# Optimization experiments

Measured on AMD Instinct MI355X. Metric: run time of the kernel, lower is better.

Reference implementation:

```python
import jax, jax.numpy as jnp
import numpy as np

NUM_NODES = 256
INPUTS = list(range(8))
OUTPUTS = list(range(248, 256))
V_MEAS = np.array(sorted(set(range(NUM_NODES)) - set(OUTPUTS)))  # 0..247
V_CORR = np.array(sorted(set(range(NUM_NODES)) - set(INPUTS)))   # 8..255
INNER_LR = 0.1
INNER_ITER = 200
B1, B2, ADAM_EPS = 0.9, 0.999, 1e-8
CAUSAL_EPS = 0.1


def _parity_loss(G, A_sub):
    # G, A_sub: [B, m, c]; enforces sum(A*G) odd
    S = jnp.sum(A_sub * G, axis=2)                 # [B, m]
    val = jnp.sin(jnp.pi * S / 2) ** 2
    return jnp.mean((val - 1.0) ** 2)


def _causal_loss(G, T):
    # T: [B, n]; penalty = relu(T_u - T_v + eps)
    T_u = T[:, V_MEAS][:, :, None]                 # [B, m, 1]
    T_v = T[:, V_CORR][:, None, :]                 # [B, 1, c]
    penalty = jax.nn.relu(T_u - T_v + CAUSAL_EPS)  # [B, m, c]
    return jnp.mean(G * penalty)


def setup_inputs() -> dict:
    key = jax.random.key(0)
    k1, k2, k3 = jax.random.split(key, 3)
    B = 128
    adj_batch = jax.random.uniform(k1, (B, NUM_NODES, NUM_NODES), dtype=jnp.float32)
    G_logits0 = jax.random.normal(k2, (B, len(V_MEAS), len(V_CORR)), dtype=jnp.float32)
    T0 = jax.random.uniform(k3, (B, NUM_NODES), dtype=jnp.float32)
    return {"adj_batch": adj_batch, "G_logits0": G_logits0, "T0": T0}


def reference(adj_batch, G_logits0, T0):
    A_sub = adj_batch[:, V_MEAS][:, :, V_CORR]     # [B, m, c]
    A_det = jax.lax.stop_gradient(A_sub)           # adj is detached in the inner loop

    def inner_loss(params):
        G_logits, T = params
        G = jax.nn.sigmoid(G_logits)
        loss_p = _parity_loss(G, A_det)
        loss_c = _causal_loss(G, T)
        loss_s = jnp.mean(jnp.abs(G - 0.5)) * 0.1
        return loss_p + loss_c + loss_s

    grad_fn = jax.grad(inner_loss)

    def adam_step(carry, t):
        params, m, v = carry
        g = grad_fn(params)
        m = jax.tree.map(lambda m_, g_: B1 * m_ + (1 - B1) * g_, m, g)
        v = jax.tree.map(lambda v_, g_: B2 * v_ + (1 - B2) * g_ * g_, v, g)
        bc1 = 1.0 - B1 ** t
        bc2 = 1.0 - B2 ** t
        params = jax.tree.map(
            lambda p, m_, v_: p - INNER_LR * (m_ / bc1) / (jnp.sqrt(v_ / bc2) + ADAM_EPS),
            params, m, v)
        return (params, m, v), None

    params0 = (G_logits0, T0)
    zeros = jax.tree.map(jnp.zeros_like, params0)
    steps = jnp.arange(1, INNER_ITER + 1, dtype=jnp.float32)
    (params, _, _), _ = jax.lax.scan(adam_step, (params0, zeros, zeros), steps)

    G_logits, T = jax.lax.stop_gradient(params)    # .detach() in torch source
    G_final = jax.nn.sigmoid(G_logits)
    final_parity = _parity_loss(G_final, A_sub)    # differentiable w.r.t. adj_batch
    final_causal = _causal_loss(G_final, T)
    return (final_parity + final_causal, final_parity, final_causal)
```

## Files before the change

kernel.cpp:

```cpp
#include <hip/hip_runtime.h>
#include <hip/hip_cooperative_groups.h>
#include <math.h>

namespace cg = cooperative_groups;

#define B_N   128
#define M_N   248
#define C_N   248
#define NODES 256
#define NT    (B_N*NODES)
#define NG    (B_N*M_N*C_N)

#define GRID  256
#define TPB   512
#define HROWS 124
#define KMAX  16

#define PI_F     3.14159265358979323846f
#define INV_BM   (1.0f/31744.0f)
#define INV_BMC  (1.0f/7872512.0f)

__device__ __forceinline__ float sigm(float x) {
    float z = expf(-fabsf(x));
    return (x >= 0.0f) ? 1.0f/(1.0f+z) : z/(1.0f+z);
}
__device__ __forceinline__ float sgn(float x) {
    return (x > 0.0f) ? 1.0f : ((x < 0.0f) ? -1.0f : 0.0f);
}

__global__ __launch_bounds__(TPB, 2) void persist_kernel(
    const float* __restrict__ adj, const float* __restrict__ Gl0,
    const float* __restrict__ T0,
    float* __restrict__ gTu,
    float* __restrict__ gTv,
    float* __restrict__ accum,
    float* __restrict__ out)
{
    __shared__ float T_lds[NODES], mT_lds[NODES], vT_lds[NODES];
    __shared__ float red[16];

    cg::grid_group grid = cg::this_grid();
    const int tid  = threadIdx.x;
    const int blkI = blockIdx.x;
    const int b    = blkI >> 1;
    const int h    = blkI & 1;
    const int wave = tid >> 6, lane = tid & 63;
    const int j0 = lane, j1 = lane+64, j2 = lane+128, j3 = lane+192;
    const bool v3 = (lane < 56);

    if (tid < NODES) {
        T_lds[tid]  = T0[b*NODES + tid];
        mT_lds[tid] = 0.0f;
        vT_lds[tid] = 0.0f;
    }

    float Gr[KMAX][4], mGr[KMAX][4], vGr[KMAX][4];
    #pragma unroll
    for (int k = 0; k < KMAX; ++k) {
        #pragma unroll
        for (int s = 0; s < 4; ++s) { Gr[k][s]=0.0f; mGr[k][s]=0.0f; vGr[k][s]=0.0f; }
        const int lr = wave + 8*k;
        if (lr < HROWS) {
            const int i = h*HROWS + lr;
            const size_t grow = ((size_t)(b*M_N + i))*C_N;
            Gr[k][0] = Gl0[grow+j0];
            Gr[k][1] = Gl0[grow+j1];
            Gr[k][2] = Gl0[grow+j2];
            if (v3) Gr[k][3] = Gl0[grow+j3];
        }
    }
    __syncthreads();

    double pw1d = 1.0, pw2d = 1.0;
    #pragma unroll 1
    for (int t = 1; t <= 200; ++t) {
        const float bc1p = (float)(1.0 - pw1d), bc2p = (float)(1.0 - pw2d);
        pw1d *= 0.9; pw2d *= 0.999;
        const float bc1 = (float)(1.0 - pw1d), bc2 = (float)(1.0 - pw2d);
        const int pw = t & 1, ps = (t-1) & 1;

        if (t > 1) {
            grid.sync();
            if (tid < NODES) {
                float g = 0.0f;
                if (tid < M_N) g += gTu[ps*(B_N*M_N) + b*M_N + tid];
                if (tid >= 8) {
                    const float* gp = gTv + (size_t)ps*(GRID*8*256)
                                    + (size_t)(b*16)*256 + (tid-8);
                    float s = 0.0f;
                    #pragma unroll
                    for (int p = 0; p < 16; ++p) s += gp[p*256];
                    g -= s;
                }
                g *= INV_BMC;
                float m_ = 0.9f*mT_lds[tid] + 0.1f*g;
                float v_ = 0.999f*vT_lds[tid] + 0.001f*(g*g);
                mT_lds[tid] = m_; vT_lds[tid] = v_;
                T_lds[tid] = T_lds[tid] - 0.1f*(m_/bc1p)/(sqrtf(v_/bc2p) + 1e-8f);
            }
            __syncthreads();
        }

        float av0 = 0.0f, av1 = 0.0f, av2 = 0.0f, av3 = 0.0f;
        #pragma unroll
        for (int k = 0; k < KMAX; ++k) {
            const int lr = wave + 8*k;
            if (lr < HROWS) {
                const int i = h*HROWS + lr;
                const size_t arow = ((size_t)(b*NODES + i))*NODES + 8;
                const float a0 = adj[arow+j0];
                const float a1 = adj[arow+j1];
                const float a2 = adj[arow+j2];
                const float a3 = v3 ? adj[arow+j3] : 0.0f;

                const float G0 = sigm(Gr[k][0]), G1 = sigm(Gr[k][1]);
                const float G2 = sigm(Gr[k][2]), G3 = sigm(Gr[k][3]);

                const float Tu = T_lds[i];
                const float d0 = Tu - T_lds[j0+8] + 0.1f;
                const float d1 = Tu - T_lds[j1+8] + 0.1f;
                const float d2 = Tu - T_lds[j2+8] + 0.1f;
                const float d3 = v3 ? (Tu - T_lds[j3+8] + 0.1f) : 0.0f;
                const float p0 = fmaxf(d0,0.0f), p1 = fmaxf(d1,0.0f);
                const float p2 = fmaxf(d2,0.0f), p3 = fmaxf(d3,0.0f);
                const float mk0 = (d0>0.0f)?1.0f:0.0f;
                const float mk1 = (d1>0.0f)?1.0f:0.0f;
                const float mk2 = (d2>0.0f)?1.0f:0.0f;
                const float mk3 = (v3 && d3>0.0f)?1.0f:0.0f;

                float sp = a0*G0 + a1*G1 + a2*G2 + (v3 ? a3*G3 : 0.0f);
                float gu = G0*mk0 + G1*mk1 + G2*mk2 + G3*mk3;
                #pragma unroll
                for (int off = 32; off > 0; off >>= 1) {
                    sp += __shfl_xor(sp, off, 64);
                    gu += __shfl_xor(gu, off, 64);
                }
                av0 += G0*mk0; av1 += G1*mk1; av2 += G2*mk2; av3 += G3*mk3;

                const float half_arg = (PI_F*sp)*0.5f;
                const float sv = sinf(half_arg), cv = cosf(half_arg);
                const float coefP = 2.0f*(sv*sv-1.0f)*sv*cv*PI_F*INV_BM;

                if (lane == 0) gTu[pw*(B_N*M_N) + b*M_N + i] = gu;

                #define DO_SLOT(Gx, ax, px, s_, valid) do { if (valid) {                 \
                    float dG  = coefP*(ax) + (px)*INV_BMC + 0.1f*INV_BMC*sgn((Gx)-0.5f); \
                    float grd = dG * (Gx) * (1.0f - (Gx));                               \
                    float m_ = 0.9f*mGr[k][s_] + 0.1f*grd;                               \
                    float v_ = 0.999f*vGr[k][s_] + 0.001f*(grd*grd);                     \
                    mGr[k][s_] = m_; vGr[k][s_] = v_;                                    \
                    Gr[k][s_] = Gr[k][s_] - 0.1f*(m_/bc1)/(sqrtf(v_/bc2)+1e-8f);         \
                } } while (0)
                DO_SLOT(G0, a0, p0, 0, true);
                DO_SLOT(G1, a1, p1, 1, true);
                DO_SLOT(G2, a2, p2, 2, true);
                DO_SLOT(G3, a3, p3, 3, v3);
                #undef DO_SLOT
            }
        }
        {
            float* gpw = gTv + (size_t)pw*(GRID*8*256) + (size_t)(blkI*8 + wave)*256;
            gpw[j0] = av0; gpw[j1] = av1; gpw[j2] = av2; gpw[j3] = av3;
        }
    }

    grid.sync();
    if (tid < NODES) {
        const float bc1p = (float)(1.0 - pw1d), bc2p = (float)(1.0 - pw2d);
        float g = 0.0f;
        if (tid < M_N) g += gTu[0*(B_N*M_N) + b*M_N + tid];
        if (tid >= 8) {
            const float* gp = gTv + (size_t)(b*16)*256 + (tid-8);
            float s = 0.0f;
            #pragma unroll
            for (int p = 0; p < 16; ++p) s += gp[p*256];
            g -= s;
        }
        g *= INV_BMC;
        float m_ = 0.9f*mT_lds[tid] + 0.1f*g;
        float v_ = 0.999f*vT_lds[tid] + 0.001f*(g*g);
        T_lds[tid] = T_lds[tid] - 0.1f*(m_/bc1p)/(sqrtf(v_/bc2p) + 1e-8f);
    }
    __syncthreads();

    float pacc = 0.0f, cacc = 0.0f;
    #pragma unroll
    for (int k = 0; k < KMAX; ++k) {
        const int lr = wave + 8*k;
        if (lr < HROWS) {
            const int i = h*HROWS + lr;
            const size_t arow = ((size_t)(b*NODES + i))*NODES + 8;
            const float a0 = adj[arow+j0];
            const float a1 = adj[arow+j1];
            const float a2 = adj[arow+j2];
            const float a3 = v3 ? adj[arow+j3] : 0.0f;
            const float G0 = sigm(Gr[k][0]), G1 = sigm(Gr[k][1]);
            const float G2 = sigm(Gr[k][2]), G3 = sigm(Gr[k][3]);
            const float Tu = T_lds[i];
            const float p0 = fmaxf(Tu - T_lds[j0+8] + 0.1f, 0.0f);
            const float p1 = fmaxf(Tu - T_lds[j1+8] + 0.1f, 0.0f);
            const float p2 = fmaxf(Tu - T_lds[j2+8] + 0.1f, 0.0f);
            const float p3 = v3 ? fmaxf(Tu - T_lds[j3+8] + 0.1f, 0.0f) : 0.0f;

            float sp = a0*G0 + a1*G1 + a2*G2 + (v3 ? a3*G3 : 0.0f);
            float cp = G0*p0 + G1*p1 + G2*p2 + (v3 ? G3*p3 : 0.0f);
            #pragma unroll
            for (int off = 32; off > 0; off >>= 1) {
                sp += __shfl_xor(sp, off, 64);
                cp += __shfl_xor(cp, off, 64);
            }
            if (lane == 0) {
                const float sv = sinf((PI_F*sp)*0.5f);
                const float dd = sv*sv - 1.0f;
                pacc += dd*dd;
                cacc += cp;
            }
        }
    }
    if (lane == 0) { red[wave] = pacc; red[8+wave] = cacc; }
    __syncthreads();
    if (tid == 0) {
        float rp = 0.0f, rc = 0.0f;
        #pragma unroll
        for (int w = 0; w < 8; ++w) { rp += red[w]; rc += red[8+w]; }
        atomicAdd(&accum[0], rp);
        atomicAdd(&accum[1], rc);
    }
    __threadfence();
    grid.sync();
    if (blkI == 0 && tid == 0) {
        const float p = __hip_atomic_load(&accum[0], __ATOMIC_RELAXED, __HIP_MEMORY_SCOPE_AGENT) * INV_BM;
        const float c = __hip_atomic_load(&accum[1], __ATOMIC_RELAXED, __HIP_MEMORY_SCOPE_AGENT) * INV_BMC;
        out[0] = p + c;
        out[1] = p;
        out[2] = c;
    }
}

#define NBLK  8
#define RPB   31

__global__ __launch_bounds__(256) void iter_kernel(
    const float* __restrict__ adj, float* __restrict__ Gl,
    float* __restrict__ mG, float* __restrict__ vG,
    float* __restrict__ T_state, float* __restrict__ mT, float* __restrict__ vT,
    float* __restrict__ gTu, float* __restrict__ gTv,
    int t, float bc1p, float bc2p, float bc1, float bc2)
{
    __shared__ float T_lds[NODES];
    __shared__ float gv_lds[4*NODES];
    const int tid = threadIdx.x;
    const int b   = blockIdx.x >> 3;
    const int blk = blockIdx.x & 7;

    if (t == 1) {
        T_lds[tid] = T_state[b*NODES + tid];
    } else {
        const int rs = t & 1, ws2 = (t+1) & 1, ps = (t-1) & 1;
        const int idx = b*NODES + tid;
        float Tval = T_state[rs*NT + idx];
        float g = 0.0f;
        if (tid < M_N) g += gTu[ps*(B_N*M_N) + b*M_N + tid];
        if (tid >= 8) {
            const float* gp = gTv + (size_t)ps*(B_N*NBLK*C_N) + (size_t)b*NBLK*C_N + (tid-8);
            float s = 0.0f;
            #pragma unroll
            for (int k = 0; k < NBLK; ++k) s += gp[k*C_N];
            g -= s;
        }
        g *= INV_BMC;
        float m_ = 0.9f*mT[rs*NT+idx] + 0.1f*g;
        float v_ = 0.999f*vT[rs*NT+idx] + 0.001f*(g*g);
        float newT = Tval - 0.1f*(m_/bc1p)/(sqrtf(v_/bc2p) + 1e-8f);
        T_state[ws2*NT+idx] = newT;
        mT[ws2*NT+idx] = m_;
        vT[ws2*NT+idx] = v_;
        T_lds[tid] = newT;
    }
    gv_lds[tid] = 0.0f; gv_lds[256+tid] = 0.0f; gv_lds[512+tid] = 0.0f; gv_lds[768+tid] = 0.0f;
    __syncthreads();

    const int wave = tid >> 6, lane = tid & 63;
    const int pw = t & 1;
    const int j0 = lane, j1 = lane+64, j2 = lane+128, j3 = lane+192;
    const bool v3 = (lane < 56);
    float av0 = 0.0f, av1 = 0.0f, av2 = 0.0f, av3 = 0.0f;

    for (int r = wave; r < RPB; r += 4) {
        const int i = blk*RPB + r;
        const size_t arow = ((size_t)(b*NODES + i))*NODES + 8;
        const size_t grow = ((size_t)(b*M_N + i))*C_N;

        float gl0 = Gl[grow+j0], gl1 = Gl[grow+j1], gl2 = Gl[grow+j2];
        float gl3 = v3 ? Gl[grow+j3] : 0.0f;
        float a0 = adj[arow+j0], a1 = adj[arow+j1], a2 = adj[arow+j2];
        float a3 = v3 ? adj[arow+j3] : 0.0f;
        float G0 = sigm(gl0), G1 = sigm(gl1), G2 = sigm(gl2), G3 = sigm(gl3);

        float Tu = T_lds[i];
        float d0 = Tu - T_lds[j0+8] + 0.1f;
        float d1 = Tu - T_lds[j1+8] + 0.1f;
        float d2 = Tu - T_lds[j2+8] + 0.1f;
        float d3 = v3 ? (Tu - T_lds[j3+8] + 0.1f) : 0.0f;
        float p0 = fmaxf(d0, 0.0f), p1 = fmaxf(d1, 0.0f);
        float p2 = fmaxf(d2, 0.0f), p3 = fmaxf(d3, 0.0f);
        float mk0 = (d0 > 0.0f) ? 1.0f : 0.0f;
        float mk1 = (d1 > 0.0f) ? 1.0f : 0.0f;
        float mk2 = (d2 > 0.0f) ? 1.0f : 0.0f;
        float mk3 = (v3 && d3 > 0.0f) ? 1.0f : 0.0f;

        float sp = a0*G0 + a1*G1 + a2*G2 + (v3 ? a3*G3 : 0.0f);
        float gu = G0*mk0 + G1*mk1 + G2*mk2 + G3*mk3;
        #pragma unroll
        for (int off = 32; off > 0; off >>= 1) {
            sp += __shfl_xor(sp, off, 64);
            gu += __shfl_xor(gu, off, 64);
        }
        av0 += G0*mk0; av1 += G1*mk1; av2 += G2*mk2; av3 += G3*mk3;

        float half_arg = (PI_F*sp)*0.5f;
        float sv = sinf(half_arg), cv = cosf(half_arg);
        float val = sv*sv;
        float coefP = 2.0f*(val-1.0f)*sv*cv*PI_F*INV_BM;

        if (lane == 0) gTu[pw*(B_N*M_N) + b*M_N + i] = gu;

        #define DO_SLOT(Gx, glx, ax, px, jx, valid) do { if (valid) {            \
            float dG  = coefP*(ax) + (px)*INV_BMC + 0.1f*INV_BMC*sgn((Gx)-0.5f); \
            float grd = dG * (Gx) * (1.0f - (Gx));                               \
            float m_ = 0.9f*mG[grow+(jx)] + 0.1f*grd;                            \
            float v_ = 0.999f*vG[grow+(jx)] + 0.001f*(grd*grd);                  \
            mG[grow+(jx)] = m_; vG[grow+(jx)] = v_;                              \
            Gl[grow+(jx)] = (glx) - 0.1f*(m_/bc1)/(sqrtf(v_/bc2)+1e-8f);         \
        } } while (0)
        DO_SLOT(G0, gl0, a0, p0, j0, true);
        DO_SLOT(G1, gl1, a1, p1, j1, true);
        DO_SLOT(G2, gl2, a2, p2, j2, true);
        DO_SLOT(G3, gl3, a3, p3, j3, v3);
        #undef DO_SLOT
    }

    gv_lds[wave*256 + j0] = av0;
    gv_lds[wave*256 + j1] = av1;
    gv_lds[wave*256 + j2] = av2;
    if (v3) gv_lds[wave*256 + j3] = av3;
    __syncthreads();
    if (tid < C_N) {
        float s = gv_lds[tid] + gv_lds[256+tid] + gv_lds[512+tid] + gv_lds[768+tid];
        gTv[(size_t)pw*(B_N*NBLK*C_N) + (size_t)(b*NBLK + blk)*C_N + tid] = s;
    }
}

__global__ __launch_bounds__(256) void t_fin_kernel(
    float* __restrict__ T_state, const float* __restrict__ mT, const float* __restrict__ vT,
    const float* __restrict__ gTu, const float* __restrict__ gTv,
    float bc1p, float bc2p)
{
    const int b = blockIdx.x, tid = threadIdx.x;
    const int idx = b*NODES + tid;
    float Tval = T_state[1*NT + idx];
    float g = 0.0f;
    if (tid < M_N) g += gTu[0*(B_N*M_N) + b*M_N + tid];
    if (tid >= 8) {
        const float* gp = gTv + (size_t)b*NBLK*C_N + (tid-8);
        float s = 0.0f;
        #pragma unroll
        for (int k = 0; k < NBLK; ++k) s += gp[k*C_N];
        g -= s;
    }
    g *= INV_BMC;
    float m_ = 0.9f*mT[1*NT+idx] + 0.1f*g;
    float v_ = 0.999f*vT[1*NT+idx] + 0.001f*(g*g);
    T_state[0*NT+idx] = Tval - 0.1f*(m_/bc1p)/(sqrtf(v_/bc2p) + 1e-8f);
}

__global__ __launch_bounds__(256) void loss_kernel(
    const float* __restrict__ adj, const float* __restrict__ Gl,
    const float* __restrict__ T_state, float* __restrict__ accum)
{
    __shared__ float T_lds[NODES];
    __shared__ float red[8];
    const int tid = threadIdx.x;
    const int b = blockIdx.x >> 3, blk = blockIdx.x & 7;
    T_lds[tid] = T_state[b*NODES + tid];
    __syncthreads();
    const int wave = tid >> 6, lane = tid & 63;
    const int j0 = lane, j1 = lane+64, j2 = lane+128, j3 = lane+192;
    const bool v3 = (lane < 56);
    float pacc = 0.0f, cacc = 0.0f;

    for (int r = wave; r < RPB; r += 4) {
        const int i = blk*RPB + r;
        const size_t arow = ((size_t)(b*NODES + i))*NODES + 8;
        const size_t grow = ((size_t)(b*M_N + i))*C_N;
        float gl0 = Gl[grow+j0], gl1 = Gl[grow+j1], gl2 = Gl[grow+j2];
        float gl3 = v3 ? Gl[grow+j3] : 0.0f;
        float a0 = adj[arow+j0], a1 = adj[arow+j1], a2 = adj[arow+j2];
        float a3 = v3 ? adj[arow+j3] : 0.0f;
        float G0 = sigm(gl0), G1 = sigm(gl1), G2 = sigm(gl2), G3 = sigm(gl3);

        float Tu = T_lds[i];
        float p0 = fmaxf(Tu - T_lds[j0+8] + 0.1f, 0.0f);
        float p1 = fmaxf(Tu - T_lds[j1+8] + 0.1f, 0.0f);
        float p2 = fmaxf(Tu - T_lds[j2+8] + 0.1f, 0.0f);
        float p3 = v3 ? fmaxf(Tu - T_lds[j3+8] + 0.1f, 0.0f) : 0.0f;

        float sp = a0*G0 + a1*G1 + a2*G2 + (v3 ? a3*G3 : 0.0f);
        float cp = G0*p0 + G1*p1 + G2*p2 + (v3 ? G3*p3 : 0.0f);
        #pragma unroll
        for (int off = 32; off > 0; off >>= 1) {
            sp += __shfl_xor(sp, off, 64);
            cp += __shfl_xor(cp, off, 64);
        }
        if (lane == 0) {
            float sv = sinf((PI_F*sp)*0.5f);
            float dd = sv*sv - 1.0f;
            pacc += dd*dd;
            cacc += cp;
        }
    }
    if (lane == 0) { red[wave] = pacc; red[4+wave] = cacc; }
    __syncthreads();
    if (tid == 0) {
        atomicAdd(&accum[0], red[0]+red[1]+red[2]+red[3]);
        atomicAdd(&accum[1], red[4]+red[5]+red[6]+red[7]);
    }
}

__global__ void finish_kernel(const float* __restrict__ accum, float* __restrict__ out) {
    if (threadIdx.x == 0 && blockIdx.x == 0) {
        float p = accum[0] / 31744.0f;
        float c = accum[1] / 7872512.0f;
        out[0] = p + c;
        out[1] = p;
        out[2] = c;
    }
}

extern "C" void kernel_launch(void* const* d_in, const int* in_sizes, int n_in,
                              void* d_out, int out_size, void* d_ws, size_t ws_size,
                              hipStream_t stream) {
    const float* adj = (const float*)d_in[0];
    float* Gl        = (float*)d_in[1];
    const float* T0  = (const float*)d_in[2];
    float* out       = (float*)d_out;
    float* ws        = (float*)d_ws;

    int dev = 0;  hipGetDevice(&dev);
    int numCU = 0;
    hipDeviceGetAttribute(&numCU, hipDeviceAttributeMultiprocessorCount, dev);
    int maxB = 0;
    hipOccupancyMaxActiveBlocksPerMultiprocessor(&maxB, persist_kernel, TPB, 0);
    const bool coop_ok = (maxB >= 1) && ((long)maxB * (long)numCU >= GRID);

    if (coop_ok) {
        float* gTu   = ws;
        float* gTv   = gTu + 2*B_N*M_N;
        float* accum = gTv + (size_t)2*GRID*8*256;
        hipMemsetAsync(accum, 0, 2*sizeof(float), stream);

        const float* Gl0 = Gl;
        void* args[] = { (void*)&adj, (void*)&Gl0, (void*)&T0,
                         (void*)&gTu, (void*)&gTv, (void*)&accum, (void*)&out };
        hipLaunchCooperativeKernel((void*)persist_kernel,
                                   dim3(GRID), dim3(TPB), args, 0, stream);
    } else {
        float* mG      = ws;
        float* vG      = mG + NG;
        float* T_state = vG + NG;
        float* mT      = T_state + 2*NT;
        float* vT      = mT + 2*NT;
        float* gTu     = vT + 2*NT;
        float* gTv     = gTu + 2*B_N*M_N;
        float* accum   = gTv + (size_t)2*B_N*NBLK*C_N;

        hipMemsetAsync(mG, 0, (size_t)2*NG*sizeof(float), stream);
        hipMemsetAsync(mT, 0, (size_t)4*NT*sizeof(float), stream);
        hipMemsetAsync(accum, 0, 2*sizeof(float), stream);
        hipMemcpyAsync(T_state, T0, NT*sizeof(float), hipMemcpyDeviceToDevice, stream);

        for (int t = 1; t <= 200; ++t) {
            float bc1p = 1.0f - (float)pow(0.9,   (double)(t-1));
            float bc2p = 1.0f - (float)pow(0.999, (double)(t-1));
            float bc1  = 1.0f - (float)pow(0.9,   (double)t);
            float bc2  = 1.0f - (float)pow(0.999, (double)t);
            iter_kernel<<<dim3(B_N*NBLK), dim3(256), 0, stream>>>(
                adj, Gl, mG, vG, T_state, mT, vT, gTu, gTv, t, bc1p, bc2p, bc1, bc2);
        }
        {
            float bc1p = 1.0f - (float)pow(0.9,   200.0);
            float bc2p = 1.0f - (float)pow(0.999, 200.0);
            t_fin_kernel<<<dim3(B_N), dim3(256), 0, stream>>>(T_state, mT, vT, gTu, gTv, bc1p, bc2p);
        }
        loss_kernel<<<dim3(B_N*NBLK), dim3(256), 0, stream>>>(adj, Gl, T_state, accum);
        finish_kernel<<<1, 64, 0, stream>>>(accum, out);
    }
}
```

Baseline: 8.113 ms.

## Move Adam second moment to LDS, vectorize column layout, use fast math intrinsics

The per-thread Adam second-moment state for G moves from registers into 128KB of dynamic LDS, which frees VGPRs so two 512-thread blocks can stay resident. Each lane now owns four contiguous columns and loads adj and G with float4, so the T_v values for those columns can be read once per step and kept. Sigmoid, sin/cos and the Adam division switch to fast intrinsics with a Newton-refined reciprocal, and blocks are remapped so that the two halves of a batch are no longer adjacent. This adds LDS traffic every step and slightly changes the numerics, and the cooperative launch now depends on the dynamic-LDS attribute being accepted.

```diff
diff --git a/kernel.cpp b/kernel.cpp
--- a/kernel.cpp
+++ b/kernel.cpp
@@ -15,11 +15,19 @@
 #define TPB   512
 #define HROWS 124
 #define KMAX  16
+#define DYN_LDS (KMAX*TPB*16)
 
 #define PI_F     3.14159265358979323846f
 #define INV_BM   (1.0f/31744.0f)
 #define INV_BMC  (1.0f/7872512.0f)
 
+__device__ __forceinline__ float rcp_nr(float x) {
+    float r = __builtin_amdgcn_rcpf(x);
+    return r * fmaf(-x, r, 2.0f);
+}
+__device__ __forceinline__ float sigm_fast(float x) {
+    return rcp_nr(1.0f + __expf(-x));
+}
 __device__ __forceinline__ float sigm(float x) {
     float z = expf(-fabsf(x));
     return (x >= 0.0f) ? 1.0f/(1.0f+z) : z/(1.0f+z);
@@ -28,7 +36,10 @@
     return (x > 0.0f) ? 1.0f : ((x < 0.0f) ? -1.0f : 0.0f);
 }
 
-__global__ __launch_bounds__(TPB, 2) void persist_kernel(
+extern __shared__ float4 vG_lds[];
+
+__global__ __launch_bounds__(TPB) __attribute__((amdgpu_waves_per_eu(2, 2)))
+void persist_kernel(
     const float* __restrict__ adj, const float* __restrict__ Gl0,
     const float* __restrict__ T0,
     float* __restrict__ gTu,
@@ -42,31 +53,31 @@
     cg::grid_group grid = cg::this_grid();
     const int tid  = threadIdx.x;
     const int blkI = blockIdx.x;
-    const int b    = blkI >> 1;
-    const int h    = blkI & 1;
+    const int b    = ((blkI >> 4) << 3) | (blkI & 7);
+    const int h    = (blkI >> 3) & 1;
     const int wave = tid >> 6, lane = tid & 63;
-    const int j0 = lane, j1 = lane+64, j2 = lane+128, j3 = lane+192;
-    const bool v3 = (lane < 56);
+    const bool v62 = (lane < 62);
+    const int jb   = v62 ? 4*lane : 0;
 
     if (tid < NODES) {
         T_lds[tid]  = T0[b*NODES + tid];
         mT_lds[tid] = 0.0f;
         vT_lds[tid] = 0.0f;
     }
-
-    float Gr[KMAX][4], mGr[KMAX][4], vGr[KMAX][4];
+    #pragma unroll
+    for (int k = 0; k < KMAX; ++k)
+        vG_lds[k*TPB + tid] = float4{0.0f, 0.0f, 0.0f, 0.0f};
+
+    float Glr[KMAX][4], mGr[KMAX][4];
     #pragma unroll
     for (int k = 0; k < KMAX; ++k) {
         #pragma unroll
-        for (int s = 0; s < 4; ++s) { Gr[k][s]=0.0f; mGr[k][s]=0.0f; vGr[k][s]=0.0f; }
+        for (int s = 0; s < 4; ++s) { Glr[k][s] = 0.0f; mGr[k][s] = 0.0f; }
         const int lr = wave + 8*k;
-        if (lr < HROWS) {
+        if (lr < HROWS && v62) {
             const int i = h*HROWS + lr;
-            const size_t grow = ((size_t)(b*M_N + i))*C_N;
-            Gr[k][0] = Gl0[grow+j0];
-            Gr[k][1] = Gl0[grow+j1];
-            Gr[k][2] = Gl0[grow+j2];
-            if (v3) Gr[k][3] = Gl0[grow+j3];
+            const float4 g4 = *(const float4*)&Gl0[((size_t)(b*M_N + i))*C_N + jb];
+            Glr[k][0] = g4.x; Glr[k][1] = g4.y; Glr[k][2] = g4.z; Glr[k][3] = g4.w;
         }
     }
     __syncthreads();
@@ -77,6 +88,7 @@
         const float bc1p = (float)(1.0 - pw1d), bc2p = (float)(1.0 - pw2d);
         pw1d *= 0.9; pw2d *= 0.999;
         const float bc1 = (float)(1.0 - pw1d), bc2 = (float)(1.0 - pw2d);
+        const float ibc1 = 1.0f/bc1, ibc2 = 1.0f/bc2;
         const int pw = t & 1, ps = (t-1) & 1;
 
         if (t > 1) {
@@ -85,7 +97,7 @@
                 float g = 0.0f;
                 if (tid < M_N) g += gTu[ps*(B_N*M_N) + b*M_N + tid];
                 if (tid >= 8) {
-                    const float* gp = gTv + (size_t)ps*(GRID*8*256)
+                    const float* gp = gTv + (size_t)ps*(B_N*16*256)
                                     + (size_t)(b*16)*256 + (tid-8);
                     float s = 0.0f;
                     #pragma unroll
@@ -101,34 +113,35 @@
             __syncthreads();
         }
 
+        const float Tv0 = T_lds[jb+8],  Tv1 = T_lds[jb+9];
+        const float Tv2 = T_lds[jb+10], Tv3 = T_lds[jb+11];
+
         float av0 = 0.0f, av1 = 0.0f, av2 = 0.0f, av3 = 0.0f;
         #pragma unroll
         for (int k = 0; k < KMAX; ++k) {
             const int lr = wave + 8*k;
             if (lr < HROWS) {
                 const int i = h*HROWS + lr;
-                const size_t arow = ((size_t)(b*NODES + i))*NODES + 8;
-                const float a0 = adj[arow+j0];
-                const float a1 = adj[arow+j1];
-                const float a2 = adj[arow+j2];
-                const float a3 = v3 ? adj[arow+j3] : 0.0f;
-
-                const float G0 = sigm(Gr[k][0]), G1 = sigm(Gr[k][1]);
-                const float G2 = sigm(Gr[k][2]), G3 = sigm(Gr[k][3]);
+                float4 a4 = {0.0f, 0.0f, 0.0f, 0.0f};
+                if (v62)
+                    a4 = *(const float4*)&adj[((size_t)(b*NODES + i))*NODES + 8 + jb];
+
+                const float G0 = sigm_fast(Glr[k][0]), G1 = sigm_fast(Glr[k][1]);
+                const float G2 = sigm_fast(Glr[k][2]), G3 = sigm_fast(Glr[k][3]);
 
                 const float Tu = T_lds[i];
-                const float d0 = Tu - T_lds[j0+8] + 0.1f;
-                const float d1 = Tu - T_lds[j1+8] + 0.1f;
-                const float d2 = Tu - T_lds[j2+8] + 0.1f;
-                const float d3 = v3 ? (Tu - T_lds[j3+8] + 0.1f) : 0.0f;
+                const float d0 = v62 ? (Tu - Tv0 + 0.1f) : 0.0f;
+                const float d1 = v62 ? (Tu - Tv1 + 0.1f) : 0.0f;
+                const float d2 = v62 ? (Tu - Tv2 + 0.1f) : 0.0f;
+                const float d3 = v62 ? (Tu - Tv3 + 0.1f) : 0.0f;
                 const float p0 = fmaxf(d0,0.0f), p1 = fmaxf(d1,0.0f);
                 const float p2 = fmaxf(d2,0.0f), p3 = fmaxf(d3,0.0f);
                 const float mk0 = (d0>0.0f)?1.0f:0.0f;
                 const float mk1 = (d1>0.0f)?1.0f:0.0f;
                 const float mk2 = (d2>0.0f)?1.0f:0.0f;
-                const float mk3 = (v3 && d3>0.0f)?1.0f:0.0f;
-
-                float sp = a0*G0 + a1*G1 + a2*G2 + (v3 ? a3*G3 : 0.0f);
+                const float mk3 = (d3>0.0f)?1.0f:0.0f;
+
+                float sp = a4.x*G0 + a4.y*G1 + a4.z*G2 + a4.w*G3;
                 float gu = G0*mk0 + G1*mk1 + G2*mk2 + G3*mk3;
                 #pragma unroll
                 for (int off = 32; off > 0; off >>= 1) {
@@ -138,29 +151,31 @@
                 av0 += G0*mk0; av1 += G1*mk1; av2 += G2*mk2; av3 += G3*mk3;
 
                 const float half_arg = (PI_F*sp)*0.5f;
-                const float sv = sinf(half_arg), cv = cosf(half_arg);
+                const float sv = __sinf(half_arg), cv = __cosf(half_arg);
                 const float coefP = 2.0f*(sv*sv-1.0f)*sv*cv*PI_F*INV_BM;
 
                 if (lane == 0) gTu[pw*(B_N*M_N) + b*M_N + i] = gu;
 
-                #define DO_SLOT(Gx, ax, px, s_, valid) do { if (valid) {                 \
+                float4 vv = vG_lds[k*TPB + tid];
+                #define DO_SLOT(Gx, ax, px, vx, s_) do {                             \
                     float dG  = coefP*(ax) + (px)*INV_BMC + 0.1f*INV_BMC*sgn((Gx)-0.5f); \
-                    float grd = dG * (Gx) * (1.0f - (Gx));                               \
-                    float m_ = 0.9f*mGr[k][s_] + 0.1f*grd;                               \
-                    float v_ = 0.999f*vGr[k][s_] + 0.001f*(grd*grd);                     \
-                    mGr[k][s_] = m_; vGr[k][s_] = v_;                                    \
-                    Gr[k][s_] = Gr[k][s_] - 0.1f*(m_/bc1)/(sqrtf(v_/bc2)+1e-8f);         \
-                } } while (0)
-                DO_SLOT(G0, a0, p0, 0, true);
-                DO_SLOT(G1, a1, p1, 1, true);
-                DO_SLOT(G2, a2, p2, 2, true);
-                DO_SLOT(G3, a3, p3, 3, v3);
+                    float grd = dG * (Gx) * (1.0f - (Gx));                           \
+                    float m_ = 0.9f*mGr[k][s_] + 0.1f*grd;                           \
+                    float v_ = 0.999f*(vx) + 0.001f*(grd*grd);                       \
+                    mGr[k][s_] = m_; (vx) = v_;                                      \
+                    Glr[k][s_] -= 0.1f*(m_*ibc1)*rcp_nr(sqrtf(v_*ibc2) + 1e-8f);     \
+                } while (0)
+                DO_SLOT(G0, a4.x, p0, vv.x, 0);
+                DO_SLOT(G1, a4.y, p1, vv.y, 1);
+                DO_SLOT(G2, a4.z, p2, vv.z, 2);
+                DO_SLOT(G3, a4.w, p3, vv.w, 3);
                 #undef DO_SLOT
+                vG_lds[k*TPB + tid] = vv;
             }
         }
         {
-            float* gpw = gTv + (size_t)pw*(GRID*8*256) + (size_t)(blkI*8 + wave)*256;
-            gpw[j0] = av0; gpw[j1] = av1; gpw[j2] = av2; gpw[j3] = av3;
+            float* gpw = gTv + (size_t)pw*(B_N*16*256) + (size_t)(b*16 + h*8 + wave)*256;
+            ((float4*)gpw)[lane] = float4{av0, av1, av2, av3};
         }
     }
 
@@ -183,41 +198,43 @@
     }
     __syncthreads();
 
-    float pacc = 0.0f, cacc = 0.0f;
-    #pragma unroll
-    for (int k = 0; k < KMAX; ++k) {
-        const int lr = wave + 8*k;
-        if (lr < HROWS) {
-            const int i = h*HROWS + lr;
-            const size_t arow = ((size_t)(b*NODES + i))*NODES + 8;
-            const float a0 = adj[arow+j0];
-            const float a1 = adj[arow+j1];
-            const float a2 = adj[arow+j2];
-            const float a3 = v3 ? adj[arow+j3] : 0.0f;
-            const float G0 = sigm(Gr[k][0]), G1 = sigm(Gr[k][1]);
-            const float G2 = sigm(Gr[k][2]), G3 = sigm(Gr[k][3]);
-            const float Tu = T_lds[i];
-            const float p0 = fmaxf(Tu - T_lds[j0+8] + 0.1f, 0.0f);
-            const float p1 = fmaxf(Tu - T_lds[j1+8] + 0.1f, 0.0f);
-            const float p2 = fmaxf(Tu - T_lds[j2+8] + 0.1f, 0.0f);
-            const float p3 = v3 ? fmaxf(Tu - T_lds[j3+8] + 0.1f, 0.0f) : 0.0f;
-
-            float sp = a0*G0 + a1*G1 + a2*G2 + (v3 ? a3*G3 : 0.0f);
-            float cp = G0*p0 + G1*p1 + G2*p2 + (v3 ? G3*p3 : 0.0f);
-            #pragma unroll
-            for (int off = 32; off > 0; off >>= 1) {
-                sp += __shfl_xor(sp, off, 64);
-                cp += __shfl_xor(cp, off, 64);
+    {
+        const float Tv0 = T_lds[jb+8],  Tv1 = T_lds[jb+9];
+        const float Tv2 = T_lds[jb+10], Tv3 = T_lds[jb+11];
+        float pacc = 0.0f, cacc = 0.0f;
+        #pragma unroll
+        for (int k = 0; k < KMAX; ++k) {
+            const int lr = wave + 8*k;
+            if (lr < HROWS) {
+                const int i = h*HROWS + lr;
+                float4 a4 = {0.0f, 0.0f, 0.0f, 0.0f};
+                if (v62)
+                    a4 = *(const float4*)&adj[((size_t)(b*NODES + i))*NODES + 8 + jb];
+                const float G0 = sigm_fast(Glr[k][0]), G1 = sigm_fast(Glr[k][1]);
+                const float G2 = sigm_fast(Glr[k][2]), G3 = sigm_fast(Glr[k][3]);
+                const float Tu = T_lds[i];
+                const float p0 = v62 ? fmaxf(Tu - Tv0 + 0.1f, 0.0f) : 0.0f;
+                const float p1 = v62 ? fmaxf(Tu - Tv1 + 0.1f, 0.0f) : 0.0f;
+                const float p2 = v62 ? fmaxf(Tu - Tv2 + 0.1f, 0.0f) : 0.0f;
+                const float p3 = v62 ? fmaxf(Tu - Tv3 + 0.1f, 0.0f) : 0.0f;
+
+                float sp = a4.x*G0 + a4.y*G1 + a4.z*G2 + a4.w*G3;
+                float cp = G0*p0 + G1*p1 + G2*p2 + G3*p3;
+                #pragma unroll
+                for (int off = 32; off > 0; off >>= 1) {
+                    sp += __shfl_xor(sp, off, 64);
+                    cp += __shfl_xor(cp, off, 64);
+                }
+                if (lane == 0) {
+                    const float sv = sinf((PI_F*sp)*0.5f);
+                    const float dd = sv*sv - 1.0f;
+                    pacc += dd*dd;
+                    cacc += cp;
+                }
             }
-            if (lane == 0) {
-                const float sv = sinf((PI_F*sp)*0.5f);
-                const float dd = sv*sv - 1.0f;
-                pacc += dd*dd;
-                cacc += cp;
-            }
-        }
-    }
-    if (lane == 0) { red[wave] = pacc; red[8+wave] = cacc; }
+        }
+        if (lane == 0) { red[wave] = pacc; red[8+wave] = cacc; }
+    }
     __syncthreads();
     if (tid == 0) {
         float rp = 0.0f, rc = 0.0f;
@@ -449,21 +466,26 @@
     int dev = 0;  hipGetDevice(&dev);
     int numCU = 0;
     hipDeviceGetAttribute(&numCU, hipDeviceAttributeMultiprocessorCount, dev);
+    hipError_t aerr = hipFuncSetAttribute((const void*)persist_kernel,
+                                          hipFuncAttributeMaxDynamicSharedMemorySize,
+                                          DYN_LDS);
     int maxB = 0;
-    hipOccupancyMaxActiveBlocksPerMultiprocessor(&maxB, persist_kernel, TPB, 0);
-    const bool coop_ok = (maxB >= 1) && ((long)maxB * (long)numCU >= GRID);
+    hipError_t oerr = hipOccupancyMaxActiveBlocksPerMultiprocessor(
+                          &maxB, persist_kernel, TPB, DYN_LDS);
+    const bool coop_ok = (aerr == hipSuccess) && (oerr == hipSuccess) &&
+                         (maxB >= 1) && ((long)maxB * (long)numCU >= GRID);
 
     if (coop_ok) {
         float* gTu   = ws;
         float* gTv   = gTu + 2*B_N*M_N;
-        float* accum = gTv + (size_t)2*GRID*8*256;
+        float* accum = gTv + (size_t)2*B_N*16*256;
         hipMemsetAsync(accum, 0, 2*sizeof(float), stream);
 
         const float* Gl0 = Gl;
         void* args[] = { (void*)&adj, (void*)&Gl0, (void*)&T0,
                          (void*)&gTu, (void*)&gTv, (void*)&accum, (void*)&out };
         hipLaunchCooperativeKernel((void*)persist_kernel,
-                                   dim3(GRID), dim3(TPB), args, 0, stream);
+                                   dim3(GRID), dim3(TPB), args, DYN_LDS, stream);
     } else {
         float* mG      = ws;
         float* vG      = mG + NG;
```

Measured after the change: 8.243 ms. Within noise of the previous version (+1.6%).
